# Kernel optimization log

Measured on AMD Instinct MI355X. Metric: run time of the kernel, lower is better.

## Reference

```python
import jax, jax.numpy as jnp
import numpy as np

NUM_GRAPHS = 256
NODES_PER_GRAPH = 64
K = 24
HID = 128

elu = jax.nn.elu


def _knn_edge_conv(x, Wc, bc):
    # x: [B*N, D]. Recompute kNN graph per graph, edge MLP, max-aggregate.
    B, N = NUM_GRAPHS, NODES_PER_GRAPH
    xg = x.reshape(B, N, -1)                       # [B, N, D]
    sq = jnp.sum(xg * xg, axis=-1)                 # [B, N]
    # squared euclidean distances within each graph: [B, N, N]
    d = sq[:, :, None] + sq[:, None, :] - 2.0 * jnp.einsum('bnd,bmd->bnm', xg, xg)
    _, idx = jax.lax.top_k(-d, K)                  # [B, N, K] nearest (incl. self)
    xj = jax.vmap(lambda g, i: g[i])(xg, idx)      # [B, N, K, D] neighbor gather
    xi = xg[:, :, None, :]                         # [B, N, 1, D]
    e = jnp.concatenate([jnp.broadcast_to(xi, xj.shape), xj - xi], axis=-1)  # [B,N,K,2D]
    m = elu(jnp.einsum('bnkf,fh->bnkh', e, Wc) + bc)
    out = jnp.max(m, axis=2)                       # max aggregation over K neighbors
    return out.reshape(B * N, -1)


def setup_inputs() -> dict:
    key = jax.random.key(0)
    ks = jax.random.split(key, 16)
    Ntot = NUM_GRAPHS * NODES_PER_GRAPH

    def w(k, fan_in, fan_out):
        return jax.random.normal(k, (fan_in, fan_out), jnp.float32) / np.sqrt(fan_in)

    return {
        'x_pf': jax.random.normal(ks[0], (Ntot, 15), jnp.float32),
        'batch_pf': jnp.repeat(jnp.arange(NUM_GRAPHS, dtype=jnp.int64 if jax.config.jax_enable_x64 else jnp.int32), NODES_PER_GRAPH),
        'W1': w(ks[1], 15, HID),  'b1': jnp.zeros((HID,), jnp.float32),
        'W2': w(ks[2], HID, HID), 'b2': jnp.zeros((HID,), jnp.float32),
        'Wc': w(ks[3], 2 * HID, HID), 'bc': jnp.zeros((HID,), jnp.float32),
        'Wo1': w(ks[4], HID, 64), 'bo1': jnp.zeros((64,), jnp.float32),
        'Wo2': w(ks[5], 64, 32),  'bo2': jnp.zeros((32,), jnp.float32),
        'Wo3': w(ks[6], 32, 32),  'bo3': jnp.zeros((32,), jnp.float32),
        'Wo4': w(ks[7], 32, 8),   'bo4': jnp.zeros((8,), jnp.float32),
    }


def reference(x_pf, batch_pf, W1, b1, W2, b2, Wc, bc, Wo1, bo1, Wo2, bo2, Wo3, bo3, Wo4, bo4):
    # pf_encode: Linear(15,128)+ELU+Linear(128,128)+ELU
    h = elu(elu(x_pf @ W1 + b1) @ W2 + b2)
    f1 = _knn_edge_conv(h, Wc, bc)
    f2 = _knn_edge_conv(f1, Wc, bc)
    f3 = _knn_edge_conv(f2, Wc, bc)
    # global_add_pool over nodes per graph
    pooled = jax.ops.segment_sum(f3, batch_pf, num_segments=NUM_GRAPHS)  # [B, 128]
    o = elu(pooled @ Wo1 + bo1)
    o = elu(o @ Wo2 + bo2)
    o = elu(o @ Wo3 + bo3)
    out = o @ Wo4 + bo4  # [B, 8]
    return (out, batch_pf)
```

## Files before the change

### kernel.cpp

```cpp
#include <hip/hip_runtime.h>
#include <hip/hip_bf16.h>
#include <hip/hip_fp16.h>
#include <math.h>

#define NG  256
#define NN  64
#define KK  24
#define HID 128
#define KP  136
#define VP  136
#define DP  68
#define FRAG 512
#define SLAB (8*4*2*FRAG)
#define HSLAB (8*4*FRAG)
#define IMG_BYTES (3*SLAB*2)

typedef __attribute__((ext_vector_type(8)))  short bf16x8;
typedef __attribute__((ext_vector_type(4)))  float f32x4;

__device__ __forceinline__ float elu1(float x){ return x > 0.f ? x : (__expf(x)-1.f); }

__device__ __forceinline__ short bf_t(float x){ return (short)(__float_as_uint(x) >> 16); }
__device__ __forceinline__ float bf_u(short s){ return __uint_as_float(((unsigned)(unsigned short)s) << 16); }

__device__ __forceinline__ short f2h(float x){ __half h = __float2half(x); return *(short*)&h; }
__device__ __forceinline__ unsigned pkmax(unsigned a, unsigned b){
    unsigned r; asm("v_pk_max_f16 %0, %1, %2" : "=v"(r) : "v"(a), "v"(b)); return r;
}
__device__ __forceinline__ float2 h22f2(unsigned u){
    __half2 h = *(__half2*)&u; return __half22float2(h);
}

extern "C" __global__ void prep_kernel(const float* __restrict__ W2,
                                       const float* __restrict__ Wc,
                                       short* __restrict__ img)
{
    int t = blockIdx.x * 256 + threadIdx.x;
    if (t >= 3*8*4*64) return;
    const int lane = t & 63;
    const int ks   = (t >> 6) & 3;
    const int tn   = (t >> 8) & 7;
    const int s    = t >> 11;
    const int n     = tn*16 + (lane & 15);
    const int kbase = ks*32 + (lane >> 4)*8;
    bf16x8 hv, lv;
    #pragma unroll
    for (int j = 0; j < 8; ++j){
        const int k = kbase + j;
        float w = (s == 0) ? W2[k*HID + n]
                : (s == 1) ? Wc[k*HID + n]
                           : Wc[(k + HID)*HID + n];
        short h = bf_t(w);
        hv[j] = h;
        lv[j] = bf_t(w - bf_u(h));
    }
    short* dst = img + s*SLAB + ((tn*4 + ks)*2)*FRAG + lane*8;
    *(bf16x8*)(dst)        = hv;
    *(bf16x8*)(dst + FRAG) = lv;
}

__device__ __forceinline__ void stage_copy(const short* __restrict__ src,
                                           short* __restrict__ slab, int tid)
{
    const uint4* s = (const uint4*)src;
    uint4* d = (uint4*)slab;
    #pragma unroll
    for (int i = 0; i < 4; ++i) d[tid + i*1024] = s[tid + i*1024];
}

__device__ __forceinline__ void stage_build(const float* __restrict__ Wg, int rowoff,
                                            short* __restrict__ slab, int tid)
{
    for (int i = tid; i < 8*4*64; i += 1024){
        const int lane2 = i & 63;
        const int ks    = (i >> 6) & 3;
        const int tn    = (i >> 8) & 7;
        const int n     = tn*16 + (lane2 & 15);
        const int kbase = ks*32 + (lane2 >> 4)*8;
        bf16x8 hv, lv;
        #pragma unroll
        for (int j = 0; j < 8; ++j){
            float w = Wg[(rowoff + kbase + j)*HID + n];
            short h = bf_t(w);
            hv[j] = h;
            lv[j] = bf_t(w - bf_u(h));
        }
        short* dst = slab + ((tn*4 + ks)*2)*FRAG + lane2*8;
        *(bf16x8*)(dst)        = hv;
        *(bf16x8*)(dst + FRAG) = lv;
    }
}

__device__ __forceinline__ void stage_hi_uv(const short* __restrict__ img,
                                            short* __restrict__ uv, int tid)
{
    const uint4* s = (const uint4*)img;
    uint4* d = (uint4*)uv;
    #pragma unroll
    for (int k = 0; k < 4; ++k){
        const int idx    = tid + k*1024;
        const int sl     = idx >> 11;
        const int within = idx & 2047;
        const int f      = within >> 6;
        const int w      = within & 63;
        d[idx] = s[(1 + sl)*4096 + f*128 + w];
    }
}

__device__ __forceinline__ void build_hi_uv(const float* __restrict__ Wc,
                                            short* __restrict__ uv, int tid)
{
    #pragma unroll
    for (int k = 0; k < 4; ++k){
        const int idx    = tid + k*1024;
        const int sl     = idx >> 11;
        const int within = idx & 2047;
        const int f      = within >> 6;
        const int lane2  = within & 63;
        const int tn = f >> 2, ks = f & 3;
        const int n     = tn*16 + (lane2 & 15);
        const int kbase = ks*32 + (lane2 >> 4)*8;
        const int rowoff = sl ? HID : 0;
        bf16x8 hv;
        #pragma unroll
        for (int j = 0; j < 8; ++j) hv[j] = bf_t(Wc[(rowoff + kbase + j)*HID + n]);
        *(bf16x8*)(uv + (size_t)idx*8) = hv;
    }
}

__device__ __forceinline__ void gemm16x2(const short* __restrict__ fbhi,
                                         const short* __restrict__ fblo,
                                         const short* __restrict__ slab,
                                         int tm, int tn0, int tn1, int lane,
                                         f32x4& c0, f32x4& c1)
{
    const int arow = tm*16 + (lane & 15);
    const int ko   = (lane >> 4) * 8;
    #pragma unroll 2
    for (int ks = 0; ks < 4; ++ks){
        bf16x8 ah = *(const bf16x8*)(fbhi + arow*KP + ks*32 + ko);
        bf16x8 al = *(const bf16x8*)(fblo + arow*KP + ks*32 + ko);
        const short* p0 = slab + ((tn0*4 + ks)*2)*FRAG + lane*8;
        const short* p1 = slab + ((tn1*4 + ks)*2)*FRAG + lane*8;
        bf16x8 bh0 = *(const bf16x8*)(p0);
        bf16x8 bl0 = *(const bf16x8*)(p0 + FRAG);
        bf16x8 bh1 = *(const bf16x8*)(p1);
        bf16x8 bl1 = *(const bf16x8*)(p1 + FRAG);
        c0 = __builtin_amdgcn_mfma_f32_16x16x32_bf16(ah, bh0, c0, 0,0,0);
        c0 = __builtin_amdgcn_mfma_f32_16x16x32_bf16(ah, bl0, c0, 0,0,0);
        c0 = __builtin_amdgcn_mfma_f32_16x16x32_bf16(al, bh0, c0, 0,0,0);
        c1 = __builtin_amdgcn_mfma_f32_16x16x32_bf16(ah, bh1, c1, 0,0,0);
        c1 = __builtin_amdgcn_mfma_f32_16x16x32_bf16(ah, bl1, c1, 0,0,0);
        c1 = __builtin_amdgcn_mfma_f32_16x16x32_bf16(al, bh1, c1, 0,0,0);
    }
}

extern "C" __global__ void __launch_bounds__(1024)
dgcnn_kernel(const float* __restrict__ x_pf,
             const float* __restrict__ W1, const float* __restrict__ b1,
             const float* __restrict__ W2, const float* __restrict__ b2,
             const float* __restrict__ Wc, const float* __restrict__ bc,
             const float* __restrict__ Wo1, const float* __restrict__ bo1,
             const float* __restrict__ Wo2, const float* __restrict__ bo2,
             const float* __restrict__ Wo3, const float* __restrict__ bo3,
             const float* __restrict__ Wo4, const float* __restrict__ bo4,
             const short* __restrict__ img, int use_img,
             float* __restrict__ out)
{
    __shared__ __align__(16) short fbhi[NN*KP];
    __shared__ __align__(16) short fblo[NN*KP];
    __shared__ __align__(16) float dmt[NN*DP];
    __shared__ __align__(16) short Vbuf16[NN*VP];
    __shared__ __align__(16) short wslab[SLAB];
    __shared__ int   knn[NN*KK];
    __shared__ float sq[NN];

    const int tid  = threadIdx.x;
    const int g    = blockIdx.x;
    const int lane = tid & 63;
    const int wv   = tid >> 6;
    const int row1 = tid >> 4;
    const int c0i  = (tid & 15) * 8;
    const int c2   = (tid & 15) * 4;

    const int t0  = wv*2, t1 = wv*2 + 1;
    const int gtm = t0 >> 3;
    const int gtn0 = t0 & 7, gtn1 = t1 & 7;

    if (tid < NN) out[NG*8 + g*NN + tid] = (float)g;

    if (use_img) stage_copy(img + 0*SLAB, wslab, tid); else stage_build(W2, 0, wslab, tid);

    {
        float acc[8];
        {
            float4 bA = *(const float4*)(b1 + c0i);
            float4 bB = *(const float4*)(b1 + c0i + 4);
            acc[0]=bA.x; acc[1]=bA.y; acc[2]=bA.z; acc[3]=bA.w;
            acc[4]=bB.x; acc[5]=bB.y; acc[6]=bB.z; acc[7]=bB.w;
        }
        #pragma unroll
        for (int f = 0; f < 15; ++f){
            float xv = x_pf[g*NN*15 + row1*15 + f];
            float4 wA = *(const float4*)(W1 + f*HID + c0i);
            float4 wB = *(const float4*)(W1 + f*HID + c0i + 4);
            acc[0] += xv*wA.x; acc[1] += xv*wA.y; acc[2] += xv*wA.z; acc[3] += xv*wA.w;
            acc[4] += xv*wB.x; acc[5] += xv*wB.y; acc[6] += xv*wB.z; acc[7] += xv*wB.w;
        }
        short4 hA, lA, hB, lB;
        float v;
        v = elu1(acc[0]); hA.x = bf_t(v); lA.x = bf_t(v - bf_u(hA.x));
        v = elu1(acc[1]); hA.y = bf_t(v); lA.y = bf_t(v - bf_u(hA.y));
        v = elu1(acc[2]); hA.z = bf_t(v); lA.z = bf_t(v - bf_u(hA.z));
        v = elu1(acc[3]); hA.w = bf_t(v); lA.w = bf_t(v - bf_u(hA.w));
        v = elu1(acc[4]); hB.x = bf_t(v); lB.x = bf_t(v - bf_u(hB.x));
        v = elu1(acc[5]); hB.y = bf_t(v); lB.y = bf_t(v - bf_u(hB.y));
        v = elu1(acc[6]); hB.z = bf_t(v); lB.z = bf_t(v - bf_u(hB.z));
        v = elu1(acc[7]); hB.w = bf_t(v); lB.w = bf_t(v - bf_u(hB.w));
        *(short4*)(fbhi + row1*KP + c0i)     = hA;
        *(short4*)(fbhi + row1*KP + c0i + 4) = hB;
        *(short4*)(fblo + row1*KP + c0i)     = lA;
        *(short4*)(fblo + row1*KP + c0i + 4) = lB;
    }
    __syncthreads();

    {
        f32x4 cA = {0,0,0,0}, cB = {0,0,0,0};
        gemm16x2(fbhi, fblo, wslab, gtm, gtn0, gtn1, lane, cA, cB);
        __syncthreads();
        #pragma unroll
        for (int half = 0; half < 2; ++half){
            const int tn  = half ? gtn1 : gtn0;
            const f32x4 c = half ? cB : cA;
            const int col = tn*16 + (lane & 15);
            const int rb  = gtm*16 + (lane >> 4)*4;
            const float bb = b2[col];
            #pragma unroll
            for (int e = 0; e < 4; ++e){
                float vv = elu1(c[e] + bb);
                short h = bf_t(vv);
                fbhi[(rb + e)*KP + col] = h;
                fblo[(rb + e)*KP + col] = bf_t(vv - bf_u(h));
            }
        }
        if (use_img) stage_hi_uv(img, wslab, tid); else build_hi_uv(Wc, wslab, tid);
    }
    __syncthreads();

    {
        bf16x8 hv = *(const bf16x8*)(fbhi + row1*KP + c0i);
        bf16x8 lv = *(const bf16x8*)(fblo + row1*KP + c0i);
        float s = 0.f;
        #pragma unroll
        for (int j = 0; j < 8; ++j){
            float vv = bf_u(hv[j]) + bf_u(lv[j]);
            s += vv*vv;
        }
        s += __shfl_xor(s, 1, 64);
        s += __shfl_xor(s, 2, 64);
        s += __shfl_xor(s, 4, 64);
        s += __shfl_xor(s, 8, 64);
        if ((tid & 15) == 0) sq[row1] = s;
    }
    __syncthreads();

    const short* Uhi = wslab;
    const short* Vhi = wslab + HSLAB;

    for (int layer = 0; layer < 3; ++layer){
        f32x4 uA = {0,0,0,0}, uB = {0,0,0,0}, vA = {0,0,0,0}, vB = {0,0,0,0};
        {
            f32x4 dc = {0.f, 0.f, 0.f, 0.f};
            const int tm0 = wv >> 2, tn0d = wv & 3;
            const int arow = tm0*16 + (lane & 15);
            const int rB   = tn0d*16 + (lane & 15);
            const int ko   = (lane >> 4) * 8;
            #pragma unroll
            for (int ks = 0; ks < 4; ++ks){
                bf16x8 ah = *(const bf16x8*)(fbhi + arow*KP + ks*32 + ko);
                bf16x8 al = *(const bf16x8*)(fblo + arow*KP + ks*32 + ko);
                bf16x8 bh = *(const bf16x8*)(fbhi + rB*KP + ks*32 + ko);
                bf16x8 bl = *(const bf16x8*)(fblo + rB*KP + ks*32 + ko);
                dc = __builtin_amdgcn_mfma_f32_16x16x32_bf16(ah, bh, dc, 0,0,0);
                dc = __builtin_amdgcn_mfma_f32_16x16x32_bf16(ah, bl, dc, 0,0,0);
                dc = __builtin_amdgcn_mfma_f32_16x16x32_bf16(al, bh, dc, 0,0,0);
                const int f0 = (gtn0*4 + ks)*FRAG + lane*8;
                const int f1 = (gtn1*4 + ks)*FRAG + lane*8;
                bf16x8 bu0 = *(const bf16x8*)(Uhi + f0);
                bf16x8 bu1 = *(const bf16x8*)(Uhi + f1);
                bf16x8 bv0 = *(const bf16x8*)(Vhi + f0);
                bf16x8 bv1 = *(const bf16x8*)(Vhi + f1);
                uA = __builtin_amdgcn_mfma_f32_16x16x32_bf16(ah, bu0, uA, 0,0,0);
                uA = __builtin_amdgcn_mfma_f32_16x16x32_bf16(al, bu0, uA, 0,0,0);
                uB = __builtin_amdgcn_mfma_f32_16x16x32_bf16(ah, bu1, uB, 0,0,0);
                uB = __builtin_amdgcn_mfma_f32_16x16x32_bf16(al, bu1, uB, 0,0,0);
                vA = __builtin_amdgcn_mfma_f32_16x16x32_bf16(ah, bv0, vA, 0,0,0);
                vA = __builtin_amdgcn_mfma_f32_16x16x32_bf16(al, bv0, vA, 0,0,0);
                vB = __builtin_amdgcn_mfma_f32_16x16x32_bf16(ah, bv1, vB, 0,0,0);
                vB = __builtin_amdgcn_mfma_f32_16x16x32_bf16(al, bv1, vB, 0,0,0);
            }
            #pragma unroll
            for (int e = 0; e < 4; ++e){
                const int ra = tm0*16 + (lane >> 4)*4 + e, ca = tn0d*16 + (lane & 15);
                dmt[ra*DP + ca] = sq[ra] + sq[ca] - 2.f*dc[e];
            }
        }
        __syncthreads();

        {
            #pragma unroll
            for (int half = 0; half < 2; ++half){
                const int tn  = half ? gtn1 : gtn0;
                const f32x4 cv = half ? vB : vA;
                const f32x4 cu = half ? uB : uA;
                const int col = tn*16 + (lane & 15);
                const int pc  = ((col & 63) << 1) + (col >> 6);
                const int rb  = gtm*16 + (lane >> 4)*4;
                #pragma unroll
                for (int e = 0; e < 4; ++e){
                    Vbuf16[(rb + e)*VP + pc] = f2h(cv[e]);
                    fbhi[(rb + e)*KP + col] = bf_t(cu[e]);
                }
            }
            #pragma unroll
            for (int p = 0; p < 4; ++p){
                const int r = wv*4 + p;
                const float dm = dmt[r*DP + lane];
                int rank = 0;
                #pragma unroll 4
                for (int q = 0; q < 16; ++q){
                    float4 v = *(const float4*)(dmt + r*DP + q*4);
                    rank += (v.x < dm) + (v.y < dm) + (v.z < dm) + (v.w < dm);
                }
                const unsigned long long mask = __ballot(rank < KK);
                if (rank < KK){
                    const int c = __popcll(mask & ((1ULL << lane) - 1ULL));
                    if (c < KK) knn[r*KK + c] = lane * (VP*2);
                }
            }
        }
        __syncthreads();

        {
            const int* kr = knn + row1*KK;
            int4 j0 = *(const int4*)(kr);
            int4 j1 = *(const int4*)(kr + 4);
            int4 j2 = *(const int4*)(kr + 8);
            int4 j3 = *(const int4*)(kr + 12);
            int4 j4 = *(const int4*)(kr + 16);
            int4 j5 = *(const int4*)(kr + 20);
            const char* Vb = (const char*)Vbuf16 + ((tid & 15) << 4);
            unsigned mx0 = 0xFC00FC00u, mx1 = 0xFC00FC00u, mx2 = 0xFC00FC00u, mx3 = 0xFC00FC00u;
            #define GM(J) { \
                uint4 v = *(const uint4*)(Vb + (J)); \
                mx0 = pkmax(mx0, v.x); mx1 = pkmax(mx1, v.y); \
                mx2 = pkmax(mx2, v.z); mx3 = pkmax(mx3, v.w); }
            GM(j0.x) GM(j0.y) GM(j0.z) GM(j0.w)
            GM(j1.x) GM(j1.y) GM(j1.z) GM(j1.w)
            GM(j2.x) GM(j2.y) GM(j2.z) GM(j2.w)
            GM(j3.x) GM(j3.y) GM(j3.z) GM(j3.w)
            GM(j4.x) GM(j4.y) GM(j4.z) GM(j4.w)
            GM(j5.x) GM(j5.y) GM(j5.z) GM(j5.w)
            #undef GM
            float2 m0 = h22f2(mx0), m1 = h22f2(mx1), m2 = h22f2(mx2), m3 = h22f2(mx3);
            uint4 sv = *(const uint4*)(Vb + row1*(VP*2));
            float2 s0 = h22f2(sv.x), s1 = h22f2(sv.y), s2 = h22f2(sv.z), s3 = h22f2(sv.w);
            float4 bcA = *(const float4*)(bc + c2);
            float4 bcB = *(const float4*)(bc + c2 + 64);
            short4 uhA = *(const short4*)(fbhi + row1*KP + c2);
            short4 uhB = *(const short4*)(fbhi + row1*KP + c2 + 64);
            float o0 = elu1(bf_u(uhA.x) - s0.x + bcA.x + m0.x);
            float o1 = elu1(bf_u(uhA.y) - s1.x + bcA.y + m1.x);
            float o2 = elu1(bf_u(uhA.z) - s2.x + bcA.z + m2.x);
            float o3 = elu1(bf_u(uhA.w) - s3.x + bcA.w + m3.x);
            float o4 = elu1(bf_u(uhB.x) - s0.y + bcB.x + m0.y);
            float o5 = elu1(bf_u(uhB.y) - s1.y + bcB.y + m1.y);
            float o6 = elu1(bf_u(uhB.z) - s2.y + bcB.z + m2.y);
            float o7 = elu1(bf_u(uhB.w) - s3.y + bcB.w + m3.y);
            short4 nhA, nlA, nhB, nlB;
            nhA.x = bf_t(o0); nlA.x = bf_t(o0 - bf_u(nhA.x));
            nhA.y = bf_t(o1); nlA.y = bf_t(o1 - bf_u(nhA.y));
            nhA.z = bf_t(o2); nlA.z = bf_t(o2 - bf_u(nhA.z));
            nhA.w = bf_t(o3); nlA.w = bf_t(o3 - bf_u(nhA.w));
            nhB.x = bf_t(o4); nlB.x = bf_t(o4 - bf_u(nhB.x));
            nhB.y = bf_t(o5); nlB.y = bf_t(o5 - bf_u(nhB.y));
            nhB.z = bf_t(o6); nlB.z = bf_t(o6 - bf_u(nhB.z));
            nhB.w = bf_t(o7); nlB.w = bf_t(o7 - bf_u(nhB.w));
            *(short4*)(fbhi + row1*KP + c2)      = nhA;
            *(short4*)(fbhi + row1*KP + c2 + 64) = nhB;
            *(short4*)(fblo + row1*KP + c2)      = nlA;
            *(short4*)(fblo + row1*KP + c2 + 64) = nlB;
            float s = o0*o0 + o1*o1 + o2*o2 + o3*o3 + o4*o4 + o5*o5 + o6*o6 + o7*o7;
            s += __shfl_xor(s, 1, 64);
            s += __shfl_xor(s, 2, 64);
            s += __shfl_xor(s, 4, 64);
            s += __shfl_xor(s, 8, 64);
            if ((tid & 15) == 0) sq[row1] = s;
        }
        __syncthreads();
    }

    float* pooled = (float*)Vbuf16;
    float* red    = pooled + 128;
    float* hr1    = pooled + 1152;
    float* hr2    = pooled + 1216;
    float* hr3    = pooled + 1248;

    {
        const int pq = tid >> 7, ch = tid & 127;
        float s = 0.f;
        for (int n = pq*8; n < pq*8 + 8; ++n)
            s += bf_u(fbhi[n*KP + ch]) + bf_u(fblo[n*KP + ch]);
        red[pq*HID + ch] = s;
    }
    __syncthreads();
    if (tid < HID){
        float s = 0.f;
        #pragma unroll
        for (int p = 0; p < 8; ++p) s += red[p*HID + tid];
        pooled[tid] = s;
    }
    __syncthreads();
    if (tid < 256){
        const int o = tid & 63, part = tid >> 6;
        float s = 0.f;
        for (int f = part*32; f < part*32 + 32; ++f) s += pooled[f] * Wo1[f*64 + o];
        red[part*64 + o] = s;
    }
    __syncthreads();
    if (tid < 64) hr1[tid] = elu1(bo1[tid] + red[tid] + red[64+tid] + red[128+tid] + red[192+tid]);
    __syncthreads();
    if (tid < 128){
        const int o = tid & 31, part = tid >> 5;
        float s = 0.f;
        for (int f = part*16; f < part*16 + 16; ++f) s += hr1[f] * Wo2[f*32 + o];
        red[part*32 + o] = s;
    }
    __syncthreads();
    if (tid < 32) hr2[tid] = elu1(bo2[tid] + red[tid] + red[32+tid] + red[64+tid] + red[96+tid]);
    __syncthreads();
    if (tid < 32){
        float a = bo3[tid];
        for (int f = 0; f < 32; ++f) a += hr2[f] * Wo3[f*32 + tid];
        hr3[tid] = elu1(a);
    }
    __syncthreads();
    if (tid < 8){
        float a = bo4[tid];
        for (int f = 0; f < 32; ++f) a += hr3[f] * Wo4[f*8 + tid];
        out[g*8 + tid] = a;
    }
}

extern "C" void kernel_launch(void* const* d_in, const int* in_sizes, int n_in,
                              void* d_out, int out_size, void* d_ws, size_t ws_size,
                              hipStream_t stream) {
    short* img = (short*)d_ws;
    const int use_img = (ws_size >= (size_t)IMG_BYTES) ? 1 : 0;
    if (use_img) {
        const int total = 3*8*4*64;
        prep_kernel<<<(total + 255)/256, 256, 0, stream>>>(
            (const float*)d_in[4], (const float*)d_in[6], img);
    }
    dgcnn_kernel<<<NG, 1024, 0, stream>>>(
        (const float*)d_in[0],
        (const float*)d_in[2],  (const float*)d_in[3],
        (const float*)d_in[4],  (const float*)d_in[5],
        (const float*)d_in[6],  (const float*)d_in[7],
        (const float*)d_in[8],  (const float*)d_in[9],
        (const float*)d_in[10], (const float*)d_in[11],
        (const float*)d_in[12], (const float*)d_in[13],
        (const float*)d_in[14], (const float*)d_in[15],
        img, use_img,
        (float*)d_out);
}
```

Before: 48.42 us.

## Drop low-part MFMAs for U/V projections and use quickselect for kNN threshold

Removes the bf16 low-part correction MFMAs from the U and V edge-projection accumulations, keeping only the high-part products. This lowers precision of the projected features. Separately, it replaces the per-lane O(64) rank counting over the distance row with a wave-wide quickselect. The quickselect uses ballot and shuffle to find the K-th smallest distance, then builds the selection mask with tie handling. The quickselect has a data-dependent iteration count, and dropping the low terms risks accuracy failures.

```diff
diff --git a/kernel.cpp b/kernel.cpp
--- a/kernel.cpp
+++ b/kernel.cpp
@@ -291,13 +291,9 @@
                 bf16x8 bv0 = *(const bf16x8*)(Vhi + f0);
                 bf16x8 bv1 = *(const bf16x8*)(Vhi + f1);
                 uA = __builtin_amdgcn_mfma_f32_16x16x32_bf16(ah, bu0, uA, 0,0,0);
-                uA = __builtin_amdgcn_mfma_f32_16x16x32_bf16(al, bu0, uA, 0,0,0);
                 uB = __builtin_amdgcn_mfma_f32_16x16x32_bf16(ah, bu1, uB, 0,0,0);
-                uB = __builtin_amdgcn_mfma_f32_16x16x32_bf16(al, bu1, uB, 0,0,0);
                 vA = __builtin_amdgcn_mfma_f32_16x16x32_bf16(ah, bv0, vA, 0,0,0);
-                vA = __builtin_amdgcn_mfma_f32_16x16x32_bf16(al, bv0, vA, 0,0,0);
                 vB = __builtin_amdgcn_mfma_f32_16x16x32_bf16(ah, bv1, vB, 0,0,0);
-                vB = __builtin_amdgcn_mfma_f32_16x16x32_bf16(al, bv1, vB, 0,0,0);
             }
             #pragma unroll
             for (int e = 0; e < 4; ++e){
@@ -326,16 +322,32 @@
             for (int p = 0; p < 4; ++p){
                 const int r = wv*4 + p;
                 const float dm = dmt[r*DP + lane];
-                int rank = 0;
-                #pragma unroll 4
-                for (int q = 0; q < 16; ++q){
-                    float4 v = *(const float4*)(dmt + r*DP + q*4);
-                    rank += (v.x < dm) + (v.y < dm) + (v.z < dm) + (v.w < dm);
+                unsigned long long cand = ~0ull;
+                float t = 0.f;
+                for (int it = 0; it < 64; ++it){
+                    const int pl = __builtin_ctzll(cand);
+                    const float pv = __shfl(dm, pl, 64);
+                    const unsigned long long lt = __ballot(dm < pv);
+                    const int c = __popcll(lt);
+                    if (c + 1 == KK){ t = pv; break; }
+                    if (c + 1 > KK) cand &= lt;
+                    else            cand &= ~(lt | (1ull << pl));
+                    if (!cand){ t = pv; break; }
                 }
-                const unsigned long long mask = __ballot(rank < KK);
-                if (rank < KK){
-                    const int c = __popcll(mask & ((1ULL << lane) - 1ULL));
-                    if (c < KK) knn[r*KK + c] = lane * (VP*2);
+                unsigned long long sel = __ballot(dm < t);
+                const int nlt = __popcll(sel);
+                int need = KK - nlt;
+                if (need > 0){
+                    unsigned long long eq = __ballot(dm == t);
+                    for (int i = 0; i < need; ++i){
+                        unsigned long long b = eq & (~eq + 1ull);
+                        if (!b) break;
+                        sel |= b; eq ^= b;
+                    }
+                }
+                if (sel & (1ull << lane)){
+                    const int idx = __popcll(sel & ((1ull << lane) - 1ull));
+                    if (idx < KK) knn[r*KK + idx] = lane * (VP*2);
                 }
             }
         }
```

Measured after the change: 53.49 us. 10.5% more time.
